# Optimization experiments

Hardware: AMD Instinct MI355X
Metric: run time of the kernel (lower is better)

Reference implementation:

```python
import jax, jax.numpy as jnp
import numpy as np

SUB_ARRAY_RATIO = 0.5
CENTER = False
EPS = 1e-8


def setup_inputs() -> dict:
    key = jax.random.key(0)
    X = jax.random.normal(key, (256, 8, 16384), dtype=jnp.float32)
    return {"X": X}


def reference(X) -> jnp.ndarray:
    # X: (N, M, T) real -> cast to complex64 (matches torch _ensure_complex)
    N, M, T = X.shape
    Xc = X - X.mean(axis=-1, keepdims=True) if CENTER else X
    Xc = Xc.astype(jnp.complex64)

    S = max(2, min(int(M * SUB_ARRAY_RATIO) + 1, M))  # sub_array_size
    J = M - S + 1                                      # number_of_sub_arrays

    # Full sample covariance C = X X^H / T, shape (N, M, M).
    # The per-window covariance R_j is just the SxS diagonal block of C at offset j,
    # so the forward-smoothed covariance is the mean of J shifted diagonal blocks.
    C = jnp.einsum("nmt,nkt->nmk", Xc, jnp.conj(Xc)) / T

    win = jnp.arange(J)[:, None] + jnp.arange(S)[None, :]  # (J, S) window row indices
    # Gather all J diagonal blocks: (N, J, S, S), then average over windows.
    R = C[:, win[:, :, None], win[:, None, :]].mean(axis=1)  # (N, S, S)

    rows, cols = jnp.triu_indices(S)
    tri = R[:, rows, cols]                                   # (N, S*(S+1)/2) complex
    feat = jnp.concatenate([tri.real, tri.imag], axis=1).astype(jnp.float32)

    mean = feat.mean(axis=1, keepdims=True)
    std = feat.std(axis=1, keepdims=True)  # correction=0, matches torch
    return (feat - mean) / (std + EPS)
```

## Files before the change

kernel.cpp:

```cpp
#include <hip/hip_runtime.h>
#include <math.h>

#define TLEN 16384
#define MROW 8
#define NPAIR 30
#define NCHUNK 8
#define NT1 256
#define EPSV 1e-8f

__global__ __launch_bounds__(NT1)
void ssf_partial(const float* __restrict__ X, float* __restrict__ part) {
    const int b   = blockIdx.x;
    const int n   = b >> 3;
    const int c   = b & 7;
    const int tid = threadIdx.x;
    const int TV  = TLEN / 4;
    const int COLS = TV / NCHUNK;
    const float4* Xv = reinterpret_cast<const float4*>(X + (size_t)n * MROW * TLEN);
    const int base = c * COLS;

    float acc[NPAIR];
#pragma unroll
    for (int p = 0; p < NPAIR; ++p) acc[p] = 0.f;

#pragma unroll
    for (int i = 0; i < COLS / NT1; ++i) {
        const int it = base + i * NT1 + tid;
        float4 x[MROW];
#pragma unroll
        for (int m = 0; m < MROW; ++m) x[m] = Xv[m * TV + it];
        const float* xv = reinterpret_cast<const float*>(x);
#pragma unroll
        for (int e = 0; e < 4; ++e) {
            int p = 0;
#pragma unroll
            for (int m = 0; m < MROW; ++m) {
                const float vm = xv[m * 4 + e];
                const int kmax = (m + 4 < MROW - 1) ? m + 4 : MROW - 1;
#pragma unroll
                for (int k = m; k <= kmax; ++k) {
                    acc[p++] += vm * xv[k * 4 + e];
                }
            }
        }
    }

#pragma unroll
    for (int p = 0; p < NPAIR; ++p) {
        float v = acc[p];
#pragma unroll
        for (int off = 32; off > 0; off >>= 1) v += __shfl_down(v, off, 64);
        acc[p] = v;
    }

    __shared__ float partial[NT1 / 64][NPAIR];
    const int wave = tid >> 6;
    const int lane = tid & 63;
    if (lane == 0) {
#pragma unroll
        for (int p = 0; p < NPAIR; ++p) partial[wave][p] = acc[p];
    }
    __syncthreads();

    if (tid < NPAIR) {
        float s = 0.f;
#pragma unroll
        for (int w = 0; w < NT1 / 64; ++w) s += partial[w][tid];
        part[(size_t)b * NPAIR + tid] = s;
    }
}

__global__ __launch_bounds__(64)
void ssf_final(const float* __restrict__ part, float* __restrict__ out) {
    const int n   = blockIdx.x;
    const int tid = threadIdx.x;
    __shared__ float Cm[MROW][MROW];

    if (tid < NPAIR) {
        float s = 0.f;
#pragma unroll
        for (int c = 0; c < NCHUNK; ++c)
            s += part[((size_t)n * NCHUNK + c) * NPAIR + tid];
        s *= (1.0f / (float)TLEN);
        int p = tid, m = 0;
        for (;;) {
            const int cnt = ((m + 4 < MROW - 1) ? m + 4 : MROW - 1) - m + 1;
            if (p < cnt) break;
            p -= cnt; ++m;
        }
        const int k = m + p;
        Cm[m][k] = s;
        Cm[k][m] = s;
    }
    __syncthreads();

    if (tid == 0) {
        const int rows[15] = {0,0,0,0,0, 1,1,1,1, 2,2,2, 3,3, 4};
        const int cols[15] = {0,1,2,3,4, 1,2,3,4, 2,3,4, 3,4, 4};
        float tri[15];
        float sum = 0.f;
#pragma unroll
        for (int i = 0; i < 15; ++i) {
            float r = 0.f;
#pragma unroll
            for (int j = 0; j < 4; ++j) r += Cm[j + rows[i]][j + cols[i]];
            r *= 0.25f;
            tri[i] = r;
            sum += r;
        }
        const float mean = sum * (1.0f / 30.0f);
        float var = 0.f;
#pragma unroll
        for (int i = 0; i < 15; ++i) { const float d = tri[i] - mean; var += d * d; }
        var += 15.0f * mean * mean;
        var *= (1.0f / 30.0f);
        const float inv = 1.0f / (sqrtf(var) + EPSV);

        float* o = out + (size_t)n * 30;
#pragma unroll
        for (int i = 0; i < 15; ++i) o[i] = (tri[i] - mean) * inv;
        const float zi = -mean * inv;
#pragma unroll
        for (int i = 0; i < 15; ++i) o[15 + i] = zi;
    }
}

extern "C" void kernel_launch(void* const* d_in, const int* in_sizes, int n_in,
                              void* d_out, int out_size, void* d_ws, size_t ws_size,
                              hipStream_t stream) {
    const float* X = (const float*)d_in[0];
    float* out  = (float*)d_out;
    float* part = (float*)d_ws;
    ssf_partial<<<256 * NCHUNK, NT1, 0, stream>>>(X, part);
    ssf_final<<<256, 64, 0, stream>>>(part, out);
}
```

Baseline: 187.8 us.

## Fuse partial covariance and finalize kernels into one block per sample

Combines the two kernels into one launch that uses a 1024-thread block per batch item. That block reduces all T columns itself and then computes the smoothed covariance features and normalization in place. This removes the second launch and the workspace round-trip. The cost is only 256 blocks instead of 2048, which cuts the parallelism available to hide memory latency on a bandwidth-bound 128MB read.

```diff
diff --git a/kernel.cpp b/kernel.cpp
--- a/kernel.cpp
+++ b/kernel.cpp
@@ -4,28 +4,23 @@
 #define TLEN 16384
 #define MROW 8
 #define NPAIR 30
-#define NCHUNK 8
-#define NT1 256
+#define NT 1024
 #define EPSV 1e-8f
 
-__global__ __launch_bounds__(NT1)
-void ssf_partial(const float* __restrict__ X, float* __restrict__ part) {
-    const int b   = blockIdx.x;
-    const int n   = b >> 3;
-    const int c   = b & 7;
+__global__ __launch_bounds__(NT, 4)
+void ssf_fused(const float* __restrict__ X, float* __restrict__ out) {
+    const int n   = blockIdx.x;
     const int tid = threadIdx.x;
     const int TV  = TLEN / 4;
-    const int COLS = TV / NCHUNK;
     const float4* Xv = reinterpret_cast<const float4*>(X + (size_t)n * MROW * TLEN);
-    const int base = c * COLS;
 
     float acc[NPAIR];
 #pragma unroll
     for (int p = 0; p < NPAIR; ++p) acc[p] = 0.f;
 
 #pragma unroll
-    for (int i = 0; i < COLS / NT1; ++i) {
-        const int it = base + i * NT1 + tid;
+    for (int i = 0; i < TV / NT; ++i) {
+        const int it = i * NT + tid;
         float4 x[MROW];
 #pragma unroll
         for (int m = 0; m < MROW; ++m) x[m] = Xv[m * TV + it];
@@ -53,7 +48,7 @@
         acc[p] = v;
     }
 
-    __shared__ float partial[NT1 / 64][NPAIR];
+    __shared__ float partial[NT / 64][NPAIR];
     const int wave = tid >> 6;
     const int lane = tid & 63;
     if (lane == 0) {
@@ -62,25 +57,11 @@
     }
     __syncthreads();
 
+    __shared__ float Cm[MROW][MROW];
     if (tid < NPAIR) {
         float s = 0.f;
 #pragma unroll
-        for (int w = 0; w < NT1 / 64; ++w) s += partial[w][tid];
-        part[(size_t)b * NPAIR + tid] = s;
-    }
-}
-
-__global__ __launch_bounds__(64)
-void ssf_final(const float* __restrict__ part, float* __restrict__ out) {
-    const int n   = blockIdx.x;
-    const int tid = threadIdx.x;
-    __shared__ float Cm[MROW][MROW];
-
-    if (tid < NPAIR) {
-        float s = 0.f;
-#pragma unroll
-        for (int c = 0; c < NCHUNK; ++c)
-            s += part[((size_t)n * NCHUNK + c) * NPAIR + tid];
+        for (int w = 0; w < NT / 64; ++w) s += partial[w][tid];
         s *= (1.0f / (float)TLEN);
         int p = tid, m = 0;
         for (;;) {
@@ -128,9 +109,8 @@
 extern "C" void kernel_launch(void* const* d_in, const int* in_sizes, int n_in,
                               void* d_out, int out_size, void* d_ws, size_t ws_size,
                               hipStream_t stream) {
+    (void)d_ws; (void)ws_size;
     const float* X = (const float*)d_in[0];
     float* out  = (float*)d_out;
-    float* part = (float*)d_ws;
-    ssf_partial<<<256 * NCHUNK, NT1, 0, stream>>>(X, part);
-    ssf_final<<<256, 64, 0, stream>>>(part, out);
+    ssf_fused<<<256, NT, 0, stream>>>(X, out);
 }
```

New measurement: 189.9 us. Within noise of the previous version (+1.1%).
